# Optimization experiments

Measured on AMD Instinct MI355X. Metric: run time of the kernel, lower is better.

## Reference

```python
import jax, jax.numpy as jnp
import numpy as np
from jax import lax

WS = 8          # window size
HEADS = 8
DIM = 192       # embed_dim == v_dim inside block
HD = DIM // HEADS
SCALE = HD ** -0.5
EPS = 1e-5


def _rel_pos_index(ws):
    coords = np.stack(np.meshgrid(np.arange(ws), np.arange(ws), indexing='ij'))  # (2,ws,ws)
    cf = coords.reshape(2, -1)                       # (2, n)
    rel = (cf[:, :, None] - cf[:, None, :]).transpose(1, 2, 0).astype(np.int64)  # (n,n,2)
    rel[..., 0] += ws - 1
    rel[..., 1] += ws - 1
    rel[..., 0] *= 2 * ws - 1
    return rel.sum(-1)                               # (n, n) int


def _ln(x, w, b):
    m = jnp.mean(x, axis=-1, keepdims=True)
    v = jnp.mean(jnp.square(x - m), axis=-1, keepdims=True)
    return (x - m) * lax.rsqrt(v + EPS) * w + b


def _conv3x3(x, w, b):
    y = lax.conv_general_dilated(x, w, (1, 1), ((1, 1), (1, 1)),
                                 dimension_numbers=('NCHW', 'OIHW', 'NCHW'))
    return y + b[None, :, None, None]


def setup_inputs():
    key = jax.random.key(0)
    ks = jax.random.split(key, 24)
    f = lambda k, shape: (jax.random.normal(k, shape, jnp.float32) * 0.02)
    inp = {
        'x': jax.random.normal(ks[0], (8, 96, 128, 128), jnp.float32),
        'v': jax.random.normal(ks[1], (8, 96, 128, 128), jnp.float32),
        'pq_w': f(ks[2], (DIM, 96, 3, 3)), 'pq_b': f(ks[3], (DIM,)),
        'pv_w': f(ks[4], (DIM, 96, 3, 3)), 'pv_b': f(ks[5], (DIM,)),
        'n1_w': jnp.ones((DIM,)), 'n1_b': jnp.zeros((DIM,)),
        'n2_w': jnp.ones((DIM,)), 'n2_b': jnp.zeros((DIM,)),
        'n3_w': jnp.ones((DIM,)), 'n3_b': jnp.zeros((DIM,)),
        'n4_w': jnp.ones((DIM,)), 'n4_b': jnp.zeros((DIM,)),
        'q_w': f(ks[6], (DIM, DIM)),
        'kv_w': f(ks[7], (2 * DIM, DIM)),
        'ap_w': f(ks[8], (DIM, DIM)), 'ap_b': f(ks[9], (DIM,)),
        'rpb': f(ks[10], ((2 * WS - 1) * (2 * WS - 1), HEADS)),
        'fc1_w': f(ks[11], (4 * DIM, DIM)), 'fc1_b': f(ks[12], (4 * DIM,)),
        'fc2_w': f(ks[13], (DIM, 4 * DIM)), 'fc2_b': f(ks[14], (DIM,)),
    }
    return inp


def reference(x, v, pq_w, pq_b, pv_w, pv_b, n1_w, n1_b, n2_w, n2_b, n3_w, n3_b,
              n4_w, n4_b, q_w, kv_w, ap_w, ap_b, rpb, fc1_w, fc1_b, fc2_w, fc2_b):
    # conv projections (input_dim != embed_dim, v_dim != embed_dim)
    x = _conv3x3(x, pq_w, pq_b)
    v = _conv3x3(v, pv_w, pv_b)
    x_proj, v_proj = x, v
    b, c, h, w = x.shape
    n = WS * WS

    xs = _ln(x.reshape(b, c, h * w).transpose(0, 2, 1), n1_w, n1_b).reshape(b, h, w, c)
    vs = _ln(v.reshape(b, c, h * w).transpose(0, 2, 1), n2_w, n2_b).reshape(b, h, w, c)

    pad_r = (WS - w % WS) % WS
    pad_b_ = (WS - h % WS) % WS
    if pad_r or pad_b_:
        xs = jnp.pad(xs, ((0, 0), (0, pad_b_), (0, pad_r), (0, 0)))
        vs = jnp.pad(vs, ((0, 0), (0, pad_b_), (0, pad_r), (0, 0)))
    hp, wp = h + pad_b_, w + pad_r

    def partition(t):  # (b,hp,wp,c) -> (nw, n, c)
        t = t.reshape(b, hp // WS, WS, wp // WS, WS, c)
        return t.transpose(0, 1, 3, 2, 4, 5).reshape(-1, n, c)

    xw = partition(xs)
    vw = partition(vs)

    # cross-window attention
    q = (xw @ q_w.T).reshape(-1, n, HEADS, HD).transpose(0, 2, 1, 3) * SCALE  # (nw,H,n,hd)
    kv = (vw @ kv_w.T).reshape(-1, n, 2, HEADS, HD).transpose(2, 0, 3, 1, 4)
    k, vv = kv[0], kv[1]                                                     # (nw,H,n,hd)
    attn = jnp.einsum('whqd,whkd->whqk', q, k)
    rel_idx = _rel_pos_index(WS)                                             # static (n,n)
    bias = rpb[rel_idx.reshape(-1)].reshape(n, n, HEADS).transpose(2, 0, 1)  # (H,n,n)
    attn = jax.nn.softmax(attn + bias[None], axis=-1)
    out = jnp.einsum('whqk,whkd->whqd', attn, vv).transpose(0, 2, 1, 3).reshape(-1, n, c)
    out = out @ ap_w.T + ap_b                                                # (nw,n,c)

    # window reverse + crop
    out = out.reshape(b, hp // WS, wp // WS, WS, WS, c).transpose(0, 1, 3, 2, 4, 5)
    out = out.reshape(b, hp, wp, c)[:, :h, :w, :].reshape(b, h * w, c)

    # mlp: note original does x = mlp(norm3(x)); x = x + drop_path(x) -> 2*mlp_out
    m = _ln(out, n3_w, n3_b)
    m = jax.nn.gelu(m @ fc1_w.T + fc1_b, approximate=False) @ fc2_w.T + fc2_b
    m = m + m
    m = _ln(m, n4_w, n4_b)
    m = m.reshape(b, h, w, c).transpose(0, 3, 1, 2)
    return m + x_proj + v_proj
```

## Files before the change

kernel.cpp:

```cpp
#include <hip/hip_runtime.h>
#include <hip/hip_bf16.h>
#include <math.h>

typedef _Float16 f16;
typedef _Float16 half8 __attribute__((ext_vector_type(8)));
typedef float f32x4 __attribute__((ext_vector_type(4)));

#define IMG 128
#define CIN 96
#define CH  192
#define SCALE_Q 0.2041241452319315f

__device__ __forceinline__ f32x4 mfma16(half8 a, half8 b, f32x4 c) {
  return __builtin_amdgcn_mfma_f32_16x16x32_f16(a, b, c, 0, 0, 0);
}

template <bool WH>
__device__ __forceinline__ half8 loadW(const void* W, int row, int k, int ldk) {
  if constexpr (WH) {
    return *(const half8*)((const f16*)W + (size_t)row * ldk + k);
  } else {
    const float* p = (const float*)W + (size_t)row * ldk + k;
    const float4 a = *(const float4*)p;
    const float4 b = *(const float4*)(p + 4);
    half8 h;
    h[0] = (f16)a.x; h[1] = (f16)a.y; h[2] = (f16)a.z; h[3] = (f16)a.w;
    h[4] = (f16)b.x; h[5] = (f16)b.y; h[6] = (f16)b.z; h[7] = (f16)b.w;
    return h;
  }
}

__device__ __forceinline__ float gelu(float x) {
  const float u = 0.70710678118654752f * x;
  const float a = fabsf(u);
  const float t = 1.0f / (1.0f + 0.3275911f * a);
  const float poly = t * (0.254829592f + t * (-0.284496736f +
                     t * (1.421413741f + t * (-1.453152027f + t * 1.061405429f))));
  float er = 1.0f - poly * __expf(-u * u);
  er = (u < 0.f) ? -er : er;
  return 0.5f * x * (1.0f + er);
}

__global__ __launch_bounds__(256) void reorder_w(
    const float* __restrict__ pq_w, const float* __restrict__ pv_w,
    const float* __restrict__ qW, const float* __restrict__ kvW,
    f16* __restrict__ Wr, f16* __restrict__ wq16) {
  const int i = blockIdx.x * 256 + threadIdx.x;
  if (i < 2 * 192 * 864) {
    const int which = i / (192 * 864);
    const int rem = i - which * (192 * 864);
    const int co = rem / 864;
    const int kk = rem - co * 864;
    const int s = kk / 96;
    const int ci = kk - s * 96;
    const float* src = which ? pv_w : pq_w;
    Wr[i] = (f16)src[co * 864 + ci * 9 + s];
  } else if (wq16) {
    const int j = i - 2 * 192 * 864;
    if (j < 110592)
      wq16[j] = (f16)(j < 36864 ? qW[j] : kvW[j - 36864]);
  }
}

__global__ __launch_bounds__(256) void reorder_w2(
    const float* __restrict__ apW, const float* __restrict__ w1,
    const float* __restrict__ w2, f16* __restrict__ dst) {
  const int i = blockIdx.x * 256 + threadIdx.x;
  if (i >= 331776) return;
  float v;
  if (i < 36864)       v = apW[i];
  else if (i < 184320) v = w1[i - 36864];
  else                 v = w2[i - 184320];
  dst[i] = (f16)v;
}

__global__ __launch_bounds__(256, 1) void conv3x3_mfma(
    const float* __restrict__ xin, const float* __restrict__ vin,
    const f16* __restrict__ Wr,
    const float* __restrict__ pq_b, const float* __restrict__ pv_b,
    f16* __restrict__ xp, f16* __restrict__ vp) {
  int bz = blockIdx.x;
  const int which = bz >> 11; bz &= 2047;
  const int b = bz >> 8;
  const int y = (bz >> 1) & 127;
  const int xseg = bz & 1;
  const int x0 = xseg * 64;
  const float* in = which ? vin : xin;
  const float* bias = which ? pv_b : pq_b;
  const f16* W = Wr + (size_t)which * 192 * 864;
  f16* out = which ? vp : xp;

  __shared__ __align__(16) f16 ST[3 * 66 * 104];
  const int tid = threadIdx.x;
  for (int i = tid; i < 3 * 96 * 66; i += 256) {
    const int r = i / (96 * 66);
    const int rem2 = i - r * (96 * 66);
    const int c = rem2 / 66;
    const int xx = rem2 - c * 66;
    const int gy = y + r - 1;
    const int gx = x0 - 1 + xx;
    float val = 0.f;
    if (gy >= 0 && gy < IMG && gx >= 0 && gx < IMG)
      val = in[(((size_t)b * CIN + c) * IMG + gy) * IMG + gx];
    ST[(r * 66 + xx) * 104 + c] = (f16)val;
  }
  __syncthreads();

  const int lane = tid & 63;
  const int wv = tid >> 6;
  const int l15 = lane & 15;
  const int quad = lane >> 4;
  const int nb = wv * 48;

  f32x4 acc[4][3];
  #pragma unroll
  for (int mt = 0; mt < 4; ++mt)
    #pragma unroll
    for (int j = 0; j < 3; ++j) acc[mt][j] = (f32x4)0.f;

  #pragma unroll
  for (int s = 0; s < 9; ++s) {
    const int ky = s / 3, kx = s - ky * 3;
    #pragma unroll
    for (int kstep = 0; kstep < 3; ++kstep) {
      const int k = kstep * 32 + quad * 8;
      half8 a[4];
      #pragma unroll
      for (int mt = 0; mt < 4; ++mt)
        a[mt] = *(const half8*)(ST + ((ky * 66) + (mt * 16 + l15) + kx) * 104 + k);
      #pragma unroll
      for (int j = 0; j < 3; ++j) {
        const half8 bf = *(const half8*)(W + (size_t)(nb + j * 16 + l15) * 864 + s * 96 + k);
        #pragma unroll
        for (int mt = 0; mt < 4; ++mt) acc[mt][j] = mfma16(a[mt], bf, acc[mt][j]);
      }
    }
  }

  const int tok0 = (b * IMG + y) * IMG + x0;
  #pragma unroll
  for (int j = 0; j < 3; ++j) {
    const int n = nb + j * 16 + l15;
    const float bn = bias[n];
    #pragma unroll
    for (int mt = 0; mt < 4; ++mt)
      #pragma unroll
      for (int reg = 0; reg < 4; ++reg) {
        const int m = mt * 16 + quad * 4 + reg;
        out[(size_t)(tok0 + m) * CH + n] = (f16)(acc[mt][j][reg] + bn);
      }
  }
}

template <bool WH>
__global__ __launch_bounds__(256, 1) void ln_qkv_mfma(
    f16* __restrict__ xp, const f16* __restrict__ vp,
    const float* __restrict__ n1w, const float* __restrict__ n1b,
    const float* __restrict__ n2w, const float* __restrict__ n2b,
    const void* __restrict__ qW, const void* __restrict__ kvW,
    f16* __restrict__ qb, f16* __restrict__ kb, f16* __restrict__ vb) {
  const int tid = threadIdx.x;
  const int lane = tid & 63;
  const int wv = tid >> 6;
  const int l15 = lane & 15;
  const int quad = lane >> 4;
  const int tok0 = blockIdx.x * 32;
  __shared__ __align__(16) f16 Ax[32 * 200];
  __shared__ __align__(16) f16 Av[32 * 200];

  {
    const int r = tid >> 3;
    const int s = tid & 7;
    const size_t gbase = (size_t)(tok0 + r) * 192 + s * 24;
    half8 hx[3], hv[3];
    const half8* px = (const half8*)(xp + gbase);
    const half8* pv = (const half8*)(vp + gbase);
    #pragma unroll
    for (int i = 0; i < 3; ++i) { hx[i] = px[i]; hv[i] = pv[i]; }
    float xv[24], vvv[24];
    float sx = 0.f, sx2 = 0.f, sv = 0.f, sv2 = 0.f;
    #pragma unroll
    for (int i = 0; i < 24; ++i) {
      xv[i] = (float)hx[i >> 3][i & 7];
      vvv[i] = (float)hv[i >> 3][i & 7];
      sx += xv[i]; sx2 += xv[i] * xv[i];
      sv += vvv[i]; sv2 += vvv[i] * vvv[i];
    }
    half8 hr[3];
    #pragma unroll
    for (int i = 0; i < 24; ++i) hr[i >> 3][i & 7] = (f16)(xv[i] + vvv[i]);
    half8* pr = (half8*)(xp + gbase);
    #pragma unroll
    for (int i = 0; i < 3; ++i) pr[i] = hr[i];
    #pragma unroll
    for (int m = 1; m < 8; m <<= 1) {
      sx += __shfl_xor(sx, m, 64); sx2 += __shfl_xor(sx2, m, 64);
      sv += __shfl_xor(sv, m, 64); sv2 += __shfl_xor(sv2, m, 64);
    }
    const float mx = sx * (1.f / 192.f);
    const float rx = rsqrtf(sx2 * (1.f / 192.f) - mx * mx + 1e-5f);
    const float mv = sv * (1.f / 192.f);
    const float rv = rsqrtf(sv2 * (1.f / 192.f) - mv * mv + 1e-5f);
    #pragma unroll
    for (int i = 0; i < 24; ++i) {
      const int c = s * 24 + i;
      Ax[r * 200 + c] = (f16)((xv[i] - mx) * rx * n1w[c] + n1b[c]);
      Av[r * 200 + c] = (f16)((vvv[i] - mv) * rv * n2w[c] + n2b[c]);
    }
  }
  __syncthreads();

  const int nb = wv * 144;
  f32x4 acc[2][9];
  #pragma unroll
  for (int mt = 0; mt < 2; ++mt)
    #pragma unroll
    for (int j = 0; j < 9; ++j) acc[mt][j] = (f32x4)0.f;

  for (int kc = 0; kc < 6; ++kc) {
    const int k = kc * 32 + quad * 8;
    const half8 ax0 = *(const half8*)(Ax + l15 * 200 + k);
    const half8 ax1 = *(const half8*)(Ax + (16 + l15) * 200 + k);
    const half8 av0 = *(const half8*)(Av + l15 * 200 + k);
    const half8 av1 = *(const half8*)(Av + (16 + l15) * 200 + k);
    #pragma unroll
    for (int j = 0; j < 9; ++j) {
      const int n0 = nb + j * 16;
      half8 b;
      if (n0 < 192) b = loadW<WH>(qW, n0 + l15, k, 192);
      else          b = loadW<WH>(kvW, n0 - 192 + l15, k, 192);
      if (n0 < 192) {
        acc[0][j] = mfma16(ax0, b, acc[0][j]);
        acc[1][j] = mfma16(ax1, b, acc[1][j]);
      } else {
        acc[0][j] = mfma16(av0, b, acc[0][j]);
        acc[1][j] = mfma16(av1, b, acc[1][j]);
      }
    }
  }

  int wro[8];
  #pragma unroll
  for (int mt = 0; mt < 2; ++mt)
    #pragma unroll
    for (int reg = 0; reg < 4; ++reg) {
      const int tok = tok0 + mt * 16 + quad * 4 + reg;
      const int bb = tok >> 14;
      const int y = (tok >> 7) & 127;
      const int xx = tok & 127;
      const int wi = bb * 256 + ((y >> 3) << 4) + (xx >> 3);
      const int t = (y & 7) * 8 + (xx & 7);
      wro[mt * 4 + reg] = wi * 12288 + t * 24;
    }
  #pragma unroll
  for (int j = 0; j < 9; ++j) {
    const int n = nb + j * 16 + l15;
    f16* dst; int c; float scale = 1.f;
    if (n < 192)      { dst = qb; c = n;       scale = SCALE_Q; }
    else if (n < 384) { dst = kb; c = n - 192; }
    else              { dst = vb; c = n - 384; }
    const int h = c / 24;
    const int cof = h * 1536 + (c - h * 24);
    #pragma unroll
    for (int mt = 0; mt < 2; ++mt)
      #pragma unroll
      for (int reg = 0; reg < 4; ++reg)
        dst[wro[mt * 4 + reg] + cof] = (f16)(acc[mt][j][reg] * scale);
  }
}

__global__ __launch_bounds__(64) void attn64(
    const f16* __restrict__ qb, const f16* __restrict__ kb,
    const f16* __restrict__ vb, const float* __restrict__ rpb,
    f16* __restrict__ fb) {
  const int wh = blockIdx.x;
  const int h = wh & 7;
  const int w = wh >> 3;
  const int t = threadIdx.x;
  __shared__ __align__(16) float ks[64 * 24];
  __shared__ __align__(16) float vs[64 * 24];
  __shared__ float bsh[225];
  const f16* kbase = kb + (size_t)wh * 1536;
  const f16* vbase = vb + (size_t)wh * 1536;
  for (int i = t; i < 1536; i += 64) { ks[i] = (float)kbase[i]; vs[i] = (float)vbase[i]; }
  for (int i = t; i < 225; i += 64) bsh[i] = rpb[i * 8 + h];
  float q[24];
  const f16* qrow = qb + ((size_t)wh * 64 + t) * 24;
  #pragma unroll
  for (int d = 0; d < 24; ++d) q[d] = (float)qrow[d];
  __syncthreads();
  const int qy = t >> 3, qx = t & 7;
  float s[64];
  float mx = -1e30f;
  #pragma unroll
  for (int kk = 0; kk < 64; ++kk) {
    float acc = 0.f;
    #pragma unroll
    for (int d = 0; d < 24; ++d) acc += q[d] * ks[kk * 24 + d];
    const int ky = kk >> 3, kx = kk & 7;
    acc += bsh[(qy - ky + 7) * 15 + (qx - kx + 7)];
    s[kk] = acc;
    mx = fmaxf(mx, acc);
  }
  float sum = 0.f;
  #pragma unroll
  for (int kk = 0; kk < 64; ++kk) { const float e = __expf(s[kk] - mx); s[kk] = e; sum += e; }
  const float inv = 1.0f / sum;
  float o[24];
  #pragma unroll
  for (int d = 0; d < 24; ++d) o[d] = 0.f;
  #pragma unroll
  for (int kk = 0; kk < 64; ++kk) {
    const float p = s[kk];
    #pragma unroll
    for (int d = 0; d < 24; ++d) o[d] += p * vs[kk * 24 + d];
  }
  f16* orow = fb + ((size_t)w * 64 + t) * 192 + h * 24;
  #pragma unroll
  for (int d = 0; d < 24; ++d) orow[d] = (f16)(o[d] * inv);
}

__global__ __launch_bounds__(256, 1) void ap_ln3_mfma(
    f16* __restrict__ fb, const f16* __restrict__ apW,
    const float* __restrict__ apb,
    const float* __restrict__ n3w, const float* __restrict__ n3b) {
  const int tid = threadIdx.x;
  const int lane = tid & 63;
  const int wv = tid >> 6;
  const int l15 = lane & 15;
  const int quad = lane >> 4;
  const int wt0 = blockIdx.x * 64;
  __shared__ __align__(16) f16 As[64 * 200];
  __shared__ float rs[64], rq[64];
  if (tid < 64) { rs[tid] = 0.f; rq[tid] = 0.f; }
  for (int i = tid; i < 64 * 24; i += 256) {
    const int r = i / 24, s = i - r * 24;
    *(half8*)(As + r * 200 + s * 8) = *(const half8*)(fb + (size_t)(wt0 + r) * 192 + s * 8);
  }
  __syncthreads();

  const int nb = wv * 48;
  f32x4 acc[4][3];
  #pragma unroll
  for (int mt = 0; mt < 4; ++mt)
    #pragma unroll
    for (int j = 0; j < 3; ++j) acc[mt][j] = (f32x4)0.f;

  for (int kc = 0; kc < 6; ++kc) {
    const int k = kc * 32 + quad * 8;
    half8 a[4];
    #pragma unroll
    for (int mt = 0; mt < 4; ++mt)
      a[mt] = *(const half8*)(As + (mt * 16 + l15) * 200 + k);
    #pragma unroll
    for (int j = 0; j < 3; ++j) {
      const half8 b = *(const half8*)(apW + (size_t)(nb + j * 16 + l15) * 192 + k);
      #pragma unroll
      for (int mt = 0; mt < 4; ++mt) acc[mt][j] = mfma16(a[mt], b, acc[mt][j]);
    }
  }
  float bias[3];
  #pragma unroll
  for (int j = 0; j < 3; ++j) bias[j] = apb[nb + j * 16 + l15];
  #pragma unroll
  for (int mt = 0; mt < 4; ++mt)
    #pragma unroll
    for (int j = 0; j < 3; ++j)
      #pragma unroll
      for (int reg = 0; reg < 4; ++reg) acc[mt][j][reg] += bias[j];

  float ssum[16], ssq[16];
  #pragma unroll
  for (int mt = 0; mt < 4; ++mt)
    #pragma unroll
    for (int reg = 0; reg < 4; ++reg) {
      const int i = mt * 4 + reg;
      const float a0 = acc[mt][0][reg], a1 = acc[mt][1][reg], a2 = acc[mt][2][reg];
      ssum[i] = a0 + a1 + a2;
      ssq[i] = a0 * a0 + a1 * a1 + a2 * a2;
    }
  #pragma unroll
  for (int m = 1; m < 16; m <<= 1)
    #pragma unroll
    for (int i = 0; i < 16; ++i) {
      ssum[i] += __shfl_xor(ssum[i], m, 64);
      ssq[i] += __shfl_xor(ssq[i], m, 64);
    }
  if (l15 == 0) {
    #pragma unroll
    for (int mt = 0; mt < 4; ++mt)
      #pragma unroll
      for (int reg = 0; reg < 4; ++reg) {
        const int row = mt * 16 + quad * 4 + reg;
        atomicAdd(&rs[row], ssum[mt * 4 + reg]);
        atomicAdd(&rq[row], ssq[mt * 4 + reg]);
      }
  }
  __syncthreads();

  float w3[3], b3[3]; int cc[3];
  #pragma unroll
  for (int j = 0; j < 3; ++j) {
    cc[j] = nb + j * 16 + l15;
    w3[j] = n3w[cc[j]]; b3[j] = n3b[cc[j]];
  }
  #pragma unroll
  for (int mt = 0; mt < 4; ++mt)
    #pragma unroll
    for (int reg = 0; reg < 4; ++reg) {
      const int row = mt * 16 + quad * 4 + reg;
      const float mean = rs[row] * (1.f / 192.f);
      const float rstd = rsqrtf(rq[row] * (1.f / 192.f) - mean * mean + 1e-5f);
      #pragma unroll
      for (int j = 0; j < 3; ++j)
        fb[(size_t)(wt0 + row) * 192 + cc[j]] =
            (f16)((acc[mt][j][reg] - mean) * rstd * w3[j] + b3[j]);
    }
}

__global__ __launch_bounds__(256, 3) void mlp_mfma(
    const f16* __restrict__ m, const f16* __restrict__ w1,
    const float* __restrict__ b1, const f16* __restrict__ w2,
    const float* __restrict__ b2,
    const float* __restrict__ n4w, const float* __restrict__ n4b,
    const f16* __restrict__ res, float* __restrict__ out) {
  const int tid = threadIdx.x;
  const int lane = tid & 63;
  const int wv = tid >> 6;
  const int l15 = lane & 15;
  const int quad = lane >> 4;
  const int wt0 = blockIdx.x * 32;
  __shared__ __align__(16) f16 SB[32 * 776];
  __shared__ float rs[32], rq[32];
  if (tid < 32) { rs[tid] = 0.f; rq[tid] = 0.f; }
  for (int i = tid; i < 32 * 24; i += 256) {
    const int r = i / 24, s = i - r * 24;
    *(half8*)(SB + r * 200 + s * 8) = *(const half8*)(m + (size_t)(wt0 + r) * 192 + s * 8);
  }
  __syncthreads();

  const int nb1 = wv * 192;
  f32x4 acc1[2][12];
  #pragma unroll
  for (int mt = 0; mt < 2; ++mt)
    #pragma unroll
    for (int j = 0; j < 12; ++j) acc1[mt][j] = (f32x4)0.f;
  for (int kc = 0; kc < 6; ++kc) {
    const int k = kc * 32 + quad * 8;
    const half8 a0 = *(const half8*)(SB + l15 * 200 + k);
    const half8 a1 = *(const half8*)(SB + (16 + l15) * 200 + k);
    #pragma unroll
    for (int j = 0; j < 12; ++j) {
      const half8 b = *(const half8*)(w1 + (size_t)(nb1 + j * 16 + l15) * 192 + k);
      acc1[0][j] = mfma16(a0, b, acc1[0][j]);
      acc1[1][j] = mfma16(a1, b, acc1[1][j]);
    }
  }
  __syncthreads();
  #pragma unroll
  for (int j = 0; j < 12; ++j) {
    const int n = nb1 + j * 16 + l15;
    const float bj = b1[n];
    #pragma unroll
    for (int mt = 0; mt < 2; ++mt)
      #pragma unroll
      for (int reg = 0; reg < 4; ++reg) {
        const int row = mt * 16 + quad * 4 + reg;
        SB[row * 776 + n] = (f16)gelu(acc1[mt][j][reg] + bj);
      }
  }
  __syncthreads();

  const int nb2 = wv * 48;
  f32x4 acc2[2][3];
  #pragma unroll
  for (int mt = 0; mt < 2; ++mt)
    #pragma unroll
    for (int j = 0; j < 3; ++j) acc2[mt][j] = (f32x4)0.f;
  for (int kc = 0; kc < 24; ++kc) {
    const int k = kc * 32 + quad * 8;
    const half8 a0 = *(const half8*)(SB + l15 * 776 + k);
    const half8 a1 = *(const half8*)(SB + (16 + l15) * 776 + k);
    #pragma unroll
    for (int j = 0; j < 3; ++j) {
      const half8 b = *(const half8*)(w2 + (size_t)(nb2 + j * 16 + l15) * 768 + k);
      acc2[0][j] = mfma16(a0, b, acc2[0][j]);
      acc2[1][j] = mfma16(a1, b, acc2[1][j]);
    }
  }
  int cc[3]; float w4[3], b4[3];
  #pragma unroll
  for (int j = 0; j < 3; ++j) {
    cc[j] = nb2 + j * 16 + l15;
    const float bj = b2[cc[j]];
    w4[j] = n4w[cc[j]]; b4[j] = n4b[cc[j]];
    #pragma unroll
    for (int mt = 0; mt < 2; ++mt)
      #pragma unroll
      for (int reg = 0; reg < 4; ++reg)
        acc2[mt][j][reg] = 2.f * (acc2[mt][j][reg] + bj);
  }
  float ssum[8], ssq[8];
  #pragma unroll
  for (int mt = 0; mt < 2; ++mt)
    #pragma unroll
    for (int reg = 0; reg < 4; ++reg) {
      const int i = mt * 4 + reg;
      const float a0 = acc2[mt][0][reg], a1 = acc2[mt][1][reg], a2 = acc2[mt][2][reg];
      ssum[i] = a0 + a1 + a2;
      ssq[i] = a0 * a0 + a1 * a1 + a2 * a2;
    }
  #pragma unroll
  for (int mm = 1; mm < 16; mm <<= 1)
    #pragma unroll
    for (int i = 0; i < 8; ++i) {
      ssum[i] += __shfl_xor(ssum[i], mm, 64);
      ssq[i] += __shfl_xor(ssq[i], mm, 64);
    }
  if (l15 == 0) {
    #pragma unroll
    for (int mt = 0; mt < 2; ++mt)
      #pragma unroll
      for (int reg = 0; reg < 4; ++reg) {
        const int row = mt * 16 + quad * 4 + reg;
        atomicAdd(&rs[row], ssum[mt * 4 + reg]);
        atomicAdd(&rq[row], ssq[mt * 4 + reg]);
      }
  }
  __syncthreads();

  const int wi = wt0 >> 6;
  const int t_base = wt0 & 63;
  const int b_img = wi >> 8;
  const int wy = (wi >> 4) & 15;
  const int wx = wi & 15;
  #pragma unroll
  for (int mt = 0; mt < 2; ++mt) {
    const int row0 = mt * 16 + quad * 4;
    const int t0 = t_base + row0;
    const int y = wy * 8 + (t0 >> 3);
    const int x0 = wx * 8 + (t0 & 7);
    float mean[4], rstd[4];
    #pragma unroll
    for (int reg = 0; reg < 4; ++reg) {
      const int row = row0 + reg;
      mean[reg] = rs[row] * (1.f / 192.f);
      rstd[reg] = rsqrtf(rq[row] * (1.f / 192.f) - mean[reg] * mean[reg] + 1e-5f);
    }
    const size_t tokbase = ((size_t)(b_img * 128 + y)) * 128 + x0;
    #pragma unroll
    for (int j = 0; j < 3; ++j) {
      float4 o;
      float vals[4];
      #pragma unroll
      for (int reg = 0; reg < 4; ++reg) {
        const float rr = (float)res[(tokbase + reg) * 192 + cc[j]];
        vals[reg] = (acc2[mt][j][reg] - mean[reg]) * rstd[reg] * w4[j] + b4[j] + rr;
      }
      o.x = vals[0]; o.y = vals[1]; o.z = vals[2]; o.w = vals[3];
      float* dst = out + ((size_t)(b_img * 192 + cc[j])) * 16384 + (y * 128 + x0);
      *(float4*)dst = o;
    }
  }
}

extern "C" void kernel_launch(void* const* d_in, const int* in_sizes, int n_in,
                              void* d_out, int out_size, void* d_ws, size_t ws_size,
                              hipStream_t stream) {
  (void)in_sizes; (void)n_in; (void)out_size;
  const float* x    = (const float*)d_in[0];
  const float* v    = (const float*)d_in[1];
  const float* pq_w = (const float*)d_in[2];
  const float* pq_b = (const float*)d_in[3];
  const float* pv_w = (const float*)d_in[4];
  const float* pv_b = (const float*)d_in[5];
  const float* n1w  = (const float*)d_in[6];
  const float* n1b  = (const float*)d_in[7];
  const float* n2w  = (const float*)d_in[8];
  const float* n2b  = (const float*)d_in[9];
  const float* n3w  = (const float*)d_in[10];
  const float* n3b  = (const float*)d_in[11];
  const float* n4w  = (const float*)d_in[12];
  const float* n4b  = (const float*)d_in[13];
  const float* qW   = (const float*)d_in[14];
  const float* kvW  = (const float*)d_in[15];
  const float* apW  = (const float*)d_in[16];
  const float* apb  = (const float*)d_in[17];
  const float* rpb  = (const float*)d_in[18];
  const float* w1   = (const float*)d_in[19];
  const float* b1   = (const float*)d_in[20];
  const float* w2   = (const float*)d_in[21];
  const float* b2   = (const float*)d_in[22];
  float* out = (float*)d_out;

  const size_t HE = 25165824;
  f16* xp   = (f16*)d_ws;
  f16* vp   = xp + HE;
  f16* vvb  = vp + HE;
  f16* qb   = (f16*)d_out;
  f16* kb   = qb + HE;
  f16* fb   = vp;
  f16* Wr   = vvb;
  f16* wtail = vvb + HE;
  const bool big = ws_size >= (3 * HE + 110592) * sizeof(f16);

  reorder_w<<<big ? 1728 : 1296, 256, 0, stream>>>(pq_w, pv_w, qW, kvW, Wr,
                                                   big ? wtail : (f16*)nullptr);
  conv3x3_mfma<<<4096, 256, 0, stream>>>(x, v, Wr, pq_b, pv_b, xp, vp);
  if (big)
    ln_qkv_mfma<true><<<4096, 256, 0, stream>>>(xp, vp, n1w, n1b, n2w, n2b,
                                                wtail, wtail + 36864, qb, kb, vvb);
  else
    ln_qkv_mfma<false><<<4096, 256, 0, stream>>>(xp, vp, n1w, n1b, n2w, n2b,
                                                 qW, kvW, qb, kb, vvb);
  attn64<<<16384, 64, 0, stream>>>(qb, kb, vvb, rpb, fb);
  reorder_w2<<<1296, 256, 0, stream>>>(apW, w1, w2, vvb);
  ap_ln3_mfma<<<2048, 256, 0, stream>>>(fb, vvb, apb, n3w, n3b);
  mlp_mfma<<<4096, 256, 0, stream>>>(fb, vvb + 36864, b1, vvb + 184320, b2,
                                     n4w, n4b, xp, out);
}
```

Measured before the change: 1.248 ms.

## Process two conv rows per block and batch weight loads ahead of MFMAs

The conv kernel now computes two output rows per block, staging a 4-row halo tile so each weight fragment feeds twice as many MFMAs, and launches half as many blocks. The qkv, attention-projection and MLP GEMM loops hoist their global weight loads into register arrays ahead of the MFMA sequence so memory latency overlaps with compute. The MLP kernel also prefetches the residual values before its second GEMM, and its launch bound drops from 3 to 2 blocks per CU. The aim is more weight reuse and better latency hiding, paid for with higher register and LDS use and possibly lower occupancy.

```diff
diff --git a/kernel.cpp b/kernel.cpp
--- a/kernel.cpp
+++ b/kernel.cpp
@@ -74,30 +74,31 @@
   dst[i] = (f16)v;
 }
 
-__global__ __launch_bounds__(256, 1) void conv3x3_mfma(
+__global__ __launch_bounds__(256, 2) void conv3x3_mfma(
     const float* __restrict__ xin, const float* __restrict__ vin,
     const f16* __restrict__ Wr,
     const float* __restrict__ pq_b, const float* __restrict__ pv_b,
     f16* __restrict__ xp, f16* __restrict__ vp) {
   int bz = blockIdx.x;
-  const int which = bz >> 11; bz &= 2047;
-  const int b = bz >> 8;
-  const int y = (bz >> 1) & 127;
+  const int which = bz >> 10; bz &= 1023;
+  const int b = bz >> 7;
+  const int yp = (bz >> 1) & 63;
   const int xseg = bz & 1;
+  const int y0 = yp * 2;
   const int x0 = xseg * 64;
   const float* in = which ? vin : xin;
   const float* bias = which ? pv_b : pq_b;
   const f16* W = Wr + (size_t)which * 192 * 864;
   f16* out = which ? vp : xp;
 
-  __shared__ __align__(16) f16 ST[3 * 66 * 104];
+  __shared__ __align__(16) f16 ST[4 * 66 * 104];
   const int tid = threadIdx.x;
-  for (int i = tid; i < 3 * 96 * 66; i += 256) {
-    const int r = i / (96 * 66);
-    const int rem2 = i - r * (96 * 66);
+  for (int i = tid; i < 4 * 96 * 66; i += 256) {
+    const int r = i / 6336;
+    const int rem2 = i - r * 6336;
     const int c = rem2 / 66;
     const int xx = rem2 - c * 66;
-    const int gy = y + r - 1;
+    const int gy = y0 + r - 1;
     const int gx = x0 - 1 + xx;
     float val = 0.f;
     if (gy >= 0 && gy < IMG && gx >= 0 && gx < IMG)
@@ -112,9 +113,9 @@
   const int quad = lane >> 4;
   const int nb = wv * 48;
 
-  f32x4 acc[4][3];
-  #pragma unroll
-  for (int mt = 0; mt < 4; ++mt)
+  f32x4 acc[8][3];
+  #pragma unroll
+  for (int mt = 0; mt < 8; ++mt)
     #pragma unroll
     for (int j = 0; j < 3; ++j) acc[mt][j] = (f32x4)0.f;
 
@@ -124,31 +125,32 @@
     #pragma unroll
     for (int kstep = 0; kstep < 3; ++kstep) {
       const int k = kstep * 32 + quad * 8;
-      half8 a[4];
-      #pragma unroll
-      for (int mt = 0; mt < 4; ++mt)
-        a[mt] = *(const half8*)(ST + ((ky * 66) + (mt * 16 + l15) + kx) * 104 + k);
+      half8 a[8];
+      #pragma unroll
+      for (int mt = 0; mt < 8; ++mt)
+        a[mt] = *(const half8*)(ST + (((mt >> 2) + ky) * 66 + (mt & 3) * 16 + l15 + kx) * 104 + k);
       #pragma unroll
       for (int j = 0; j < 3; ++j) {
         const half8 bf = *(const half8*)(W + (size_t)(nb + j * 16 + l15) * 864 + s * 96 + k);
         #pragma unroll
-        for (int mt = 0; mt < 4; ++mt) acc[mt][j] = mfma16(a[mt], bf, acc[mt][j]);
+        for (int mt = 0; mt < 8; ++mt) acc[mt][j] = mfma16(a[mt], bf, acc[mt][j]);
       }
     }
   }
 
-  const int tok0 = (b * IMG + y) * IMG + x0;
   #pragma unroll
   for (int j = 0; j < 3; ++j) {
     const int n = nb + j * 16 + l15;
     const float bn = bias[n];
     #pragma unroll
-    for (int mt = 0; mt < 4; ++mt)
-      #pragma unroll
-      for (int reg = 0; reg < 4; ++reg) {
-        const int m = mt * 16 + quad * 4 + reg;
-        out[(size_t)(tok0 + m) * CH + n] = (f16)(acc[mt][j][reg] + bn);
-      }
+    for (int mt = 0; mt < 8; ++mt) {
+      const int row = y0 + (mt >> 2);
+      const int px = x0 + (mt & 3) * 16 + quad * 4;
+      const int tok = (b * IMG + row) * IMG + px;
+      #pragma unroll
+      for (int reg = 0; reg < 4; ++reg)
+        out[(size_t)(tok + reg) * CH + n] = (f16)(acc[mt][j][reg] + bn);
+    }
   }
 }
 
@@ -219,6 +221,13 @@
 
   for (int kc = 0; kc < 6; ++kc) {
     const int k = kc * 32 + quad * 8;
+    half8 wb[9];
+    #pragma unroll
+    for (int j = 0; j < 9; ++j) {
+      const int n0 = nb + j * 16;
+      if (n0 < 192) wb[j] = loadW<WH>(qW, n0 + l15, k, 192);
+      else          wb[j] = loadW<WH>(kvW, n0 - 192 + l15, k, 192);
+    }
     const half8 ax0 = *(const half8*)(Ax + l15 * 200 + k);
     const half8 ax1 = *(const half8*)(Ax + (16 + l15) * 200 + k);
     const half8 av0 = *(const half8*)(Av + l15 * 200 + k);
@@ -226,15 +235,12 @@
     #pragma unroll
     for (int j = 0; j < 9; ++j) {
       const int n0 = nb + j * 16;
-      half8 b;
-      if (n0 < 192) b = loadW<WH>(qW, n0 + l15, k, 192);
-      else          b = loadW<WH>(kvW, n0 - 192 + l15, k, 192);
       if (n0 < 192) {
-        acc[0][j] = mfma16(ax0, b, acc[0][j]);
-        acc[1][j] = mfma16(ax1, b, acc[1][j]);
+        acc[0][j] = mfma16(ax0, wb[j], acc[0][j]);
+        acc[1][j] = mfma16(ax1, wb[j], acc[1][j]);
       } else {
-        acc[0][j] = mfma16(av0, b, acc[0][j]);
-        acc[1][j] = mfma16(av1, b, acc[1][j]);
+        acc[0][j] = mfma16(av0, wb[j], acc[0][j]);
+        acc[1][j] = mfma16(av1, wb[j], acc[1][j]);
       }
     }
   }
@@ -346,17 +352,27 @@
     #pragma unroll
     for (int j = 0; j < 3; ++j) acc[mt][j] = (f32x4)0.f;
 
-  for (int kc = 0; kc < 6; ++kc) {
-    const int k = kc * 32 + quad * 8;
-    half8 a[4];
-    #pragma unroll
-    for (int mt = 0; mt < 4; ++mt)
-      a[mt] = *(const half8*)(As + (mt * 16 + l15) * 200 + k);
-    #pragma unroll
-    for (int j = 0; j < 3; ++j) {
-      const half8 b = *(const half8*)(apW + (size_t)(nb + j * 16 + l15) * 192 + k);
-      #pragma unroll
-      for (int mt = 0; mt < 4; ++mt) acc[mt][j] = mfma16(a[mt], b, acc[mt][j]);
+  #pragma unroll
+  for (int g = 0; g < 2; ++g) {
+    half8 wb[3][3];
+    #pragma unroll
+    for (int u = 0; u < 3; ++u) {
+      const int k = (g * 3 + u) * 32 + quad * 8;
+      #pragma unroll
+      for (int j = 0; j < 3; ++j)
+        wb[u][j] = *(const half8*)(apW + (size_t)(nb + j * 16 + l15) * 192 + k);
+    }
+    #pragma unroll
+    for (int u = 0; u < 3; ++u) {
+      const int k = (g * 3 + u) * 32 + quad * 8;
+      half8 a[4];
+      #pragma unroll
+      for (int mt = 0; mt < 4; ++mt)
+        a[mt] = *(const half8*)(As + (mt * 16 + l15) * 200 + k);
+      #pragma unroll
+      for (int j = 0; j < 3; ++j)
+        #pragma unroll
+        for (int mt = 0; mt < 4; ++mt) acc[mt][j] = mfma16(a[mt], wb[u][j], acc[mt][j]);
     }
   }
   float bias[3];
@@ -418,7 +434,7 @@
     }
 }
 
-__global__ __launch_bounds__(256, 3) void mlp_mfma(
+__global__ __launch_bounds__(256, 2) void mlp_mfma(
     const f16* __restrict__ m, const f16* __restrict__ w1,
     const float* __restrict__ b1, const f16* __restrict__ w2,
     const float* __restrict__ b2,
@@ -447,13 +463,16 @@
     for (int j = 0; j < 12; ++j) acc1[mt][j] = (f32x4)0.f;
   for (int kc = 0; kc < 6; ++kc) {
     const int k = kc * 32 + quad * 8;
+    half8 wb[12];
+    #pragma unroll
+    for (int j = 0; j < 12; ++j)
+      wb[j] = *(const half8*)(w1 + (size_t)(nb1 + j * 16 + l15) * 192 + k);
     const half8 a0 = *(const half8*)(SB + l15 * 200 + k);
     const half8 a1 = *(const half8*)(SB + (16 + l15) * 200 + k);
     #pragma unroll
     for (int j = 0; j < 12; ++j) {
-      const half8 b = *(const half8*)(w1 + (size_t)(nb1 + j * 16 + l15) * 192 + k);
-      acc1[0][j] = mfma16(a0, b, acc1[0][j]);
-      acc1[1][j] = mfma16(a1, b, acc1[1][j]);
+      acc1[0][j] = mfma16(a0, wb[j], acc1[0][j]);
+      acc1[1][j] = mfma16(a1, wb[j], acc1[1][j]);
     }
   }
   __syncthreads();
@@ -472,26 +491,57 @@
   __syncthreads();
 
   const int nb2 = wv * 48;
+  int cc[3];
+  #pragma unroll
+  for (int j = 0; j < 3; ++j) cc[j] = nb2 + j * 16 + l15;
+  const int wi = wt0 >> 6;
+  const int t_base = wt0 & 63;
+  const int b_img = wi >> 8;
+  const int wy = (wi >> 4) & 15;
+  const int wx = wi & 15;
+  float rr[2][3][4];
+  #pragma unroll
+  for (int mt = 0; mt < 2; ++mt) {
+    const int t0 = t_base + mt * 16 + quad * 4;
+    const int y = wy * 8 + (t0 >> 3);
+    const int xx0 = wx * 8 + (t0 & 7);
+    const size_t tokbase = ((size_t)(b_img * 128 + y)) * 128 + xx0;
+    #pragma unroll
+    for (int j = 0; j < 3; ++j)
+      #pragma unroll
+      for (int reg = 0; reg < 4; ++reg)
+        rr[mt][j][reg] = (float)res[(tokbase + reg) * 192 + cc[j]];
+  }
+
   f32x4 acc2[2][3];
   #pragma unroll
   for (int mt = 0; mt < 2; ++mt)
     #pragma unroll
     for (int j = 0; j < 3; ++j) acc2[mt][j] = (f32x4)0.f;
-  for (int kc = 0; kc < 24; ++kc) {
-    const int k = kc * 32 + quad * 8;
-    const half8 a0 = *(const half8*)(SB + l15 * 776 + k);
-    const half8 a1 = *(const half8*)(SB + (16 + l15) * 776 + k);
-    #pragma unroll
-    for (int j = 0; j < 3; ++j) {
-      const half8 b = *(const half8*)(w2 + (size_t)(nb2 + j * 16 + l15) * 768 + k);
-      acc2[0][j] = mfma16(a0, b, acc2[0][j]);
-      acc2[1][j] = mfma16(a1, b, acc2[1][j]);
-    }
-  }
-  int cc[3]; float w4[3], b4[3];
+  for (int g = 0; g < 6; ++g) {
+    half8 wb[4][3];
+    #pragma unroll
+    for (int u = 0; u < 4; ++u) {
+      const int k = (g * 4 + u) * 32 + quad * 8;
+      #pragma unroll
+      for (int j = 0; j < 3; ++j)
+        wb[u][j] = *(const half8*)(w2 + (size_t)(nb2 + j * 16 + l15) * 768 + k);
+    }
+    #pragma unroll
+    for (int u = 0; u < 4; ++u) {
+      const int k = (g * 4 + u) * 32 + quad * 8;
+      const half8 a0 = *(const half8*)(SB + l15 * 776 + k);
+      const half8 a1 = *(const half8*)(SB + (16 + l15) * 776 + k);
+      #pragma unroll
+      for (int j = 0; j < 3; ++j) {
+        acc2[0][j] = mfma16(a0, wb[u][j], acc2[0][j]);
+        acc2[1][j] = mfma16(a1, wb[u][j], acc2[1][j]);
+      }
+    }
+  }
+  float w4[3], b4[3];
   #pragma unroll
   for (int j = 0; j < 3; ++j) {
-    cc[j] = nb2 + j * 16 + l15;
     const float bj = b2[cc[j]];
     w4[j] = n4w[cc[j]]; b4[j] = n4b[cc[j]];
     #pragma unroll
@@ -529,11 +579,6 @@
   }
   __syncthreads();
 
-  const int wi = wt0 >> 6;
-  const int t_base = wt0 & 63;
-  const int b_img = wi >> 8;
-  const int wy = (wi >> 4) & 15;
-  const int wx = wi & 15;
   #pragma unroll
   for (int mt = 0; mt < 2; ++mt) {
     const int row0 = mt * 16 + quad * 4;
@@ -547,16 +592,13 @@
       mean[reg] = rs[row] * (1.f / 192.f);
       rstd[reg] = rsqrtf(rq[row] * (1.f / 192.f) - mean[reg] * mean[reg] + 1e-5f);
     }
-    const size_t tokbase = ((size_t)(b_img * 128 + y)) * 128 + x0;
     #pragma unroll
     for (int j = 0; j < 3; ++j) {
       float4 o;
       float vals[4];
       #pragma unroll
-      for (int reg = 0; reg < 4; ++reg) {
-        const float rr = (float)res[(tokbase + reg) * 192 + cc[j]];
-        vals[reg] = (acc2[mt][j][reg] - mean[reg]) * rstd[reg] * w4[j] + b4[j] + rr;
-      }
+      for (int reg = 0; reg < 4; ++reg)
+        vals[reg] = (acc2[mt][j][reg] - mean[reg]) * rstd[reg] * w4[j] + b4[j] + rr[mt][j][reg];
       o.x = vals[0]; o.y = vals[1]; o.z = vals[2]; o.w = vals[3];
       float* dst = out + ((size_t)(b_img * 192 + cc[j])) * 16384 + (y * 128 + x0);
       *(float4*)dst = o;
@@ -606,7 +648,7 @@
 
   reorder_w<<<big ? 1728 : 1296, 256, 0, stream>>>(pq_w, pv_w, qW, kvW, Wr,
                                                    big ? wtail : (f16*)nullptr);
-  conv3x3_mfma<<<4096, 256, 0, stream>>>(x, v, Wr, pq_b, pv_b, xp, vp);
+  conv3x3_mfma<<<2048, 256, 0, stream>>>(x, v, Wr, pq_b, pv_b, xp, vp);
   if (big)
     ln_qkv_mfma<true><<<4096, 256, 0, stream>>>(xp, vp, n1w, n1b, n2w, n2b,
                                                 wtail, wtail + 36864, qb, kb, vvb);
```

Result: faster. 1.176 ms (-5.7%).
